# Kernel optimization log

Hardware: AMD Instinct MI355X
Metric: run time of the kernel (lower is better)

## Reference

```python
import jax, jax.numpy as jnp
import numpy as np

B, N, C, H = 16, 1024, 768, 12
GRID = 32  # 32x32 patch grid -> N = 1024 tokens
ROPE_BASE = 10000.0


def setup_inputs() -> dict:
    key = jax.random.key(0)
    k1, k2, k3 = jax.random.split(key, 3)
    x = jax.random.normal(k1, (B, N, C), dtype=jnp.float32)
    W_qkv = jax.random.normal(k2, (C, 3 * C), dtype=jnp.float32) * 0.02
    b_qkv = jnp.zeros((3 * C,), dtype=jnp.float32)
    W_proj = jax.random.normal(k3, (C, C), dtype=jnp.float32) * 0.02
    b_proj = jnp.zeros((C,), dtype=jnp.float32)
    ids = jnp.arange(N)
    pos_h = jnp.broadcast_to(ids // GRID, (B, N)).astype(jnp.int32)
    pos_w = jnp.broadcast_to(ids % GRID, (B, N)).astype(jnp.int32)
    return dict(x=x, W_qkv=W_qkv, b_qkv=b_qkv, W_proj=W_proj, b_proj=b_proj,
                pos_h=pos_h, pos_w=pos_w, num_heads=H)


def _rotate_half(t):
    t1, t2 = jnp.split(t, 2, axis=-1)
    return jnp.concatenate((-t2, t1), axis=-1)


def _rope_1d(t, pos, inv):
    # t: (B,H,N,d_rope), pos: (B,N), inv: (d_rope//2,)
    p = pos.astype(jnp.float32)[..., None] * inv      # (B,N,d_rope//2)
    p = p[:, None]                                    # (B,1,N,d_rope//2)
    cos = jnp.repeat(jnp.cos(p), 2, axis=-1)          # repeat_interleave(2)
    sin = jnp.repeat(jnp.sin(p), 2, axis=-1)
    return t * cos + _rotate_half(t) * sin


def reference(x, W_qkv, b_qkv, W_proj, b_proj, pos_h, pos_w, num_heads):
    Bx, Nx, Cx = x.shape
    hd = Cx // num_heads
    d_rope = hd // 2
    inv = 1.0 / ROPE_BASE ** (jnp.arange(0, d_rope, 2, dtype=jnp.float32) / float(max(d_rope, 1)))
    qkv = (x @ W_qkv + b_qkv).reshape(Bx, Nx, 3, num_heads, hd).transpose(2, 0, 3, 1, 4)
    q, k, v = qkv[0], qkv[1], qkv[2]                  # each (B,H,N,hd)
    # 2D RoPE: row-half / col-half of head_dim
    qh, qw = jnp.split(q, 2, axis=-1)
    kh, kw = jnp.split(k, 2, axis=-1)
    qh = _rope_1d(qh, pos_h, inv); kh = _rope_1d(kh, pos_h, inv)
    qw = _rope_1d(qw, pos_w, inv); kw = _rope_1d(kw, pos_w, inv)
    q = jnp.concatenate((qh, qw), axis=-1)
    k = jnp.concatenate((kh, kw), axis=-1)
    scale = hd ** -0.5
    attn = jax.nn.softmax(jnp.einsum('bhnd,bhmd->bhnm', q, k) * scale, axis=-1)
    out = jnp.einsum('bhnm,bhmd->bhnd', attn, v).transpose(0, 2, 1, 3).reshape(Bx, Nx, Cx)
    return out @ W_proj + b_proj
```

## Files before the change

### kernel.cpp

```cpp
#include <hip/hip_runtime.h>
#include <hip/hip_bf16.h>

#define B_ 16
#define N_ 1024
#define C_ 768
#define H_ 12
#define HD_ 64
#define QC_ (3*C_)

using bf16 = __hip_bfloat16;
using bf16x8 = __attribute__((ext_vector_type(8))) __bf16;
using f32x4  = __attribute__((ext_vector_type(4))) float;

__device__ __forceinline__ float tof(bf16 v){ return __bfloat162float(v); }

__device__ __forceinline__ void gload16(const void* g, void* l) {
  __builtin_amdgcn_global_load_lds(
      (const __attribute__((address_space(1))) unsigned int*)g,
      (__attribute__((address_space(3))) unsigned int*)l, 16, 0, 0);
}

__device__ __forceinline__ int xcd_swizzle(int bid, int nwg) {
  return (bid & 7) * (nwg >> 3) + (bid >> 3);
}

__device__ __forceinline__ unsigned pk2(float a, float b) {
  unsigned ua = (unsigned)__bfloat16_as_ushort(__float2bfloat16(a));
  unsigned ub = (unsigned)__bfloat16_as_ushort(__float2bfloat16(b));
  return ua | (ub << 16);
}

__global__ __launch_bounds__(256) void detect_dtype(
    const unsigned* __restrict__ x32, int* __restrict__ flag)
{
  __shared__ int cnt;
  if (threadIdx.x == 0) cnt = 0;
  __syncthreads();
  int local = 0;
  #pragma unroll
  for (int i = 0; i < 16; i++) {
    unsigned u = x32[threadIdx.x * 16 + i * 4096];
    unsigned e = (u >> 7) & 0xFF;
    local += (e >= 110 && e <= 140) ? 1 : 0;
  }
  atomicAdd(&cnt, local);
  __syncthreads();
  if (threadIdx.x == 0) *flag = (cnt > 2048) ? 1 : 0;
}

__global__ __launch_bounds__(256) void cvt_x(
    const void* __restrict__ x, bf16* __restrict__ xb,
    const int* __restrict__ flag, const int n4, const int off4)
{
  const int i = blockIdx.x * 256 + threadIdx.x;
  if (i >= n4) return;
  if (*flag) {
    ((uint2*)xb)[i] = ((const uint2*)x)[off4 + i];
  } else {
    float4 v = ((const float4*)x)[off4 + i];
    xb[i*4+0] = __float2bfloat16(v.x);
    xb[i*4+1] = __float2bfloat16(v.y);
    xb[i*4+2] = __float2bfloat16(v.z);
    xb[i*4+3] = __float2bfloat16(v.w);
  }
}

__global__ __launch_bounds__(256) void wt_cvt(
    const void* __restrict__ W, bf16* __restrict__ WT,
    const int K, const int Nd, const int* __restrict__ flag)
{
  __shared__ float t[32][33];
  const int fl = *flag;
  const int n0 = blockIdx.x * 32, k0 = blockIdx.y * 32;
  const int tx = threadIdx.x & 31, ty = threadIdx.x >> 5;
  for (int kk = ty; kk < 32; kk += 8) {
    const size_t gi = (size_t)(k0 + kk) * Nd + (n0 + tx);
    t[kk][tx] = fl ? tof(((const bf16*)W)[gi]) : ((const float*)W)[gi];
  }
  __syncthreads();
  for (int nn = ty; nn < 32; nn += 8)
    WT[(size_t)(n0 + nn) * K + (k0 + tx)] = __float2bfloat16(t[tx][nn]);
}

__global__ __launch_bounds__(256) void gemm_qkv_rope(
    const bf16* __restrict__ Ab, const bf16* __restrict__ WT,
    const void* __restrict__ bias, bf16* __restrict__ Qp,
    bf16* __restrict__ Kp, bf16* __restrict__ Vtb,
    const int* __restrict__ flag,
    const int* __restrict__ pos_h, const int* __restrict__ pos_w)
{
  const int K = C_;
  const bool bbf = (*flag != 0);

  __shared__ __align__(16) char smem[36864];
  unsigned short* As = (unsigned short*)smem;
  unsigned short* Bs = (unsigned short*)(smem + 16384);

  const int tid = threadIdx.x;
  const int l   = tid & 63;
  const int w   = tid >> 6;
  const int wm  = (w & 1) * 64;
  const int wn  = (w >> 1) * 64;

  const int nwg = gridDim.x * gridDim.y;
  const int bid = blockIdx.y * gridDim.x + blockIdx.x;
  const int lb  = xcd_swizzle(bid, nwg);
  const int gy  = gridDim.y;
  const int brow = lb / gy;
  const int bcol = lb - brow * gy;
  const int row0 = brow * 128;
  const int col0 = bcol * 128;

  const int srow = w*8 + (l >> 3);
  const int sch  = (l & 7) ^ (l >> 3);
  const bf16* Ast = Ab + (size_t)(row0 + srow) * K + sch * 8;
  const bf16* Bst = WT + (size_t)(col0 + srow) * K + sch * 8;

  f32x4 acc[4][4] = {};

  for (int k0 = 0; k0 < K; k0 += 64) {
    __syncthreads();
    #pragma unroll
    for (int i = 0; i < 4; i++) {
      gload16(Ast + (size_t)i*32*K + k0, As + (i*32 + w*8)*64);
      gload16(Bst + (size_t)i*32*K + k0, Bs + (i*32 + w*8)*64);
    }
    __syncthreads();
    #pragma unroll
    for (int s = 0; s < 2; s++) {
      bf16x8 af[4], bg[4];
      const int ch = (s*4 + (l >> 4)) ^ (l & 7);
      #pragma unroll
      for (int i = 0; i < 4; i++) {
        const int rowm = wm + i*16 + (l & 15);
        const int rown = wn + i*16 + (l & 15);
        af[i] = *(const bf16x8*)&As[rowm*64 + ch*8];
        bg[i] = *(const bf16x8*)&Bs[rown*64 + ch*8];
      }
      #pragma unroll
      for (int i = 0; i < 4; i++)
        #pragma unroll
        for (int j = 0; j < 4; j++)
          acc[i][j] = __builtin_amdgcn_mfma_f32_16x16x32_bf16(
                          af[i], bg[j], acc[i][j], 0, 0, 0);
    }
  }

  const int colbase = col0 + wn;
  const int t   = colbase / 768;
  const int h   = (colbase % 768) >> 6;
  const int dd0 = l & 15;
  float bv4[4];
  #pragma unroll
  for (int j = 0; j < 4; j++) {
    const int c = colbase + dd0 + j*16;
    bv4[j] = bbf ? tof(((const bf16*)bias)[c]) : ((const float*)bias)[c];
  }
  const int rb = row0 + wm + (l >> 4) * 4;

  __syncthreads();
  bf16* Ts = (bf16*)(smem + w * 9216);

  if (t == 2) {
    #pragma unroll
    for (int i = 0; i < 4; i++) {
      #pragma unroll
      for (int v = 0; v < 4; v++) {
        const int nl = i*16 + ((l >> 4) << 2) + v;
        #pragma unroll
        for (int j = 0; j < 4; j++) {
          const int dl = dd0 + j*16;
          const float y = acc[i][j][v] + bv4[j];
          Ts[dl*72 + (((nl >> 3) ^ (dl & 7)) << 3) + (nl & 7)] =
              __float2bfloat16(y);
        }
      }
    }
  } else {
    const int fi  = dd0 >> 1;
    const float LOG2B = 13.287712379549449f;
    const float f1 = exp2f(-LOG2B * (float)fi       * (1.0f/16.0f));
    const float f2 = exp2f(-LOG2B * (float)(fi + 8) * (1.0f/16.0f));
    #pragma unroll
    for (int i = 0; i < 4; i++) {
      #pragma unroll
      for (int v = 0; v < 4; v++) {
        const int r  = rb + i*16 + v;
        const int rl = i*16 + (l >> 4)*4 + v;
        float y0 = acc[i][0][v] + bv4[0];
        float y1 = acc[i][1][v] + bv4[1];
        float y2 = acc[i][2][v] + bv4[2];
        float y3 = acc[i][3][v] + bv4[3];
        const float ph = (float)pos_h[r];
        const float pw = (float)pos_w[r];
        float s1,c1,s2,c2,s3,c3,s4,c4;
        __sincosf(ph*f1, &s1, &c1);
        __sincosf(ph*f2, &s2, &c2);
        __sincosf(pw*f1, &s3, &c3);
        __sincosf(pw*f2, &s4, &c4);
        float z[4];
        z[0] = y0*c1 - y1*s1;
        z[1] = y1*c2 + y0*s2;
        z[2] = y2*c3 - y3*s3;
        z[3] = y3*c4 + y2*s4;
        if (t == 0) {
          const float QS = 0.18033688011112042f;
          z[0]*=QS; z[1]*=QS; z[2]*=QS; z[3]*=QS;
        }
        #pragma unroll
        for (int j = 0; j < 4; j++) {
          const int cl = dd0 + j*16;
          Ts[rl*72 + (((cl >> 3) ^ (rl & 7)) << 3) + (cl & 7)] =
              __float2bfloat16(z[j]);
        }
      }
    }
  }
  __syncthreads();

  if (t == 2) {
    const int n0 = (row0 + wm) & 1023;
    const int bp = (row0 + wm) >> 10;
    const size_t gbase = (size_t)(bp*12 + h) * 65536;
    #pragma unroll
    for (int dr = 0; dr < 8; dr++) {
      const int dl = dr*8 + (l >> 3);
      const int c  = l & 7;
      uint4 vv = *(const uint4*)&Ts[dl*72 + ((c ^ (dl & 7)) << 3)];
      *(uint4*)&Vtb[gbase + (size_t)dl*1024 + n0 + c*8] = vv;
    }
  } else {
    bf16* dst = (t == 0) ? Qp : Kp;
    const int rg0 = row0 + wm;
    const int bp  = rg0 >> 10;
    const int nb  = rg0 & 1023;
    const size_t gbase = (size_t)(bp*12 + h) * 65536;
    #pragma unroll
    for (int dr = 0; dr < 8; dr++) {
      const int rl = dr*8 + (l >> 3);
      const int c  = l & 7;
      uint4 vv = *(const uint4*)&Ts[rl*72 + ((c ^ (rl & 7)) << 3)];
      *(uint4*)&dst[gbase + (size_t)(nb + rl)*64 + c*8] = vv;
    }
  }
}

__global__ __launch_bounds__(256) void attn_mfma(
    const bf16* __restrict__ Qp, const bf16* __restrict__ Kp,
    const bf16* __restrict__ Vtb, bf16* __restrict__ ao)
{
  __shared__ __align__(16) bf16 QPs[64*64];
  __shared__ __align__(16) bf16 Ks[64*64];
  __shared__ __align__(16) bf16 Vs[64*64];
  bf16* Qs = QPs;
  bf16* Ps = QPs;
  const int tid = threadIdx.x;
  const int l   = tid & 63;
  const int w   = tid >> 6;

  const int nwg = gridDim.x * gridDim.y;
  const int bid = blockIdx.y * gridDim.x + blockIdx.x;
  const int lb  = xcd_swizzle(bid, nwg);
  const int qt  = lb & 15;
  const int bh  = lb >> 4;
  const size_t base = (size_t)bh * 65536;

  const int srow = w*8 + (l >> 3);
  const int sch  = (l & 7) ^ (l >> 3);
  const bf16* Qst = Qp  + base + (size_t)(qt*64 + srow)*64 + sch*8;
  const bf16* Kst = Kp  + base + (size_t)srow*64   + sch*8;
  const bf16* Vst = Vtb + base + (size_t)srow*1024 + sch*8;

  #pragma unroll
  for (int i = 0; i < 2; i++)
    gload16(Qst + (size_t)i*32*64, Qs + (i*32 + w*8)*64);
  __syncthreads();

  bf16x8 af[2];
  {
    const int row = w*16 + (l & 15);
    #pragma unroll
    for (int s = 0; s < 2; s++) {
      const int ch = (s*4 + (l >> 4)) ^ (row & 7);
      af[s] = *(const bf16x8*)&Qs[row*64 + ch*8];
    }
  }

  bf16x8 ones;
  #pragma unroll
  for (int i = 0; i < 8; i++) ones[i] = (__bf16)1.0f;

  float m_i = -3.0e38f;
  f32x4 l_acc = {};
  f32x4 o[4] = {};

  const int g    = l >> 4;
  const int qrow = w*16 + (l & 15);

  for (int kt = 0; kt < 16; kt++) {
    __syncthreads();
    #pragma unroll
    for (int i = 0; i < 2; i++) {
      gload16(Kst + (size_t)(kt*64 + i*32)*64, Ks + (i*32 + w*8)*64);
      gload16(Vst + (size_t)i*32*1024 + kt*64, Vs + (i*32 + w*8)*64);
    }
    __syncthreads();

    f32x4 s[4];
    __builtin_amdgcn_s_setprio(1);
    #pragma unroll
    for (int nt = 0; nt < 4; nt++) {
      f32x4 a = {};
      const int nrow = nt*16 + (l & 15);
      #pragma unroll
      for (int ss = 0; ss < 2; ss++) {
        const int ch = (ss*4 + (l >> 4)) ^ (nrow & 7);
        bf16x8 bg = *(const bf16x8*)&Ks[nrow*64 + ch*8];
        a = __builtin_amdgcn_mfma_f32_16x16x32_bf16(bg, af[ss], a, 0, 0, 0);
      }
      s[nt] = a;
    }
    __builtin_amdgcn_s_setprio(0);

    float a0 = fmaxf(fmaxf(s[0][0], s[0][1]), s[0][2]);
    float a1 = fmaxf(fmaxf(s[0][3], s[1][0]), s[1][1]);
    float a2 = fmaxf(fmaxf(s[1][2], s[1][3]), s[2][0]);
    float a3 = fmaxf(fmaxf(s[2][1], s[2][2]), s[2][3]);
    float a4 = fmaxf(fmaxf(s[3][0], s[3][1]), s[3][2]);
    float b0 = fmaxf(fmaxf(a0, a1), a2);
    float b1 = fmaxf(fmaxf(a3, a4), s[3][3]);
    float mloc = fmaxf(b0, b1);
    mloc = fmaxf(mloc, __shfl_xor(mloc, 16));
    const float m0 = fmaxf(mloc, __shfl_xor(mloc, 32));

    if (!__all(m0 - m_i <= 8.0f)) {
      const float mx = fmaxf(m_i, m0);
      const float alpha = exp2f(m_i - mx);
      m_i = mx;
      float a_o[4];
      #pragma unroll
      for (int v = 0; v < 4; v++)
        a_o[v] = __shfl(alpha, (l & 48) | ((g << 2) + v));
      #pragma unroll
      for (int v = 0; v < 4; v++) {
        l_acc[v] *= a_o[v];
        #pragma unroll
        for (int nt = 0; nt < 4; nt++) o[nt][v] *= a_o[v];
      }
    }

    #pragma unroll
    for (int nt = 0; nt < 4; nt++) {
      const float p0 = exp2f(s[nt][0] - m_i);
      const float p1 = exp2f(s[nt][1] - m_i);
      const float p2 = exp2f(s[nt][2] - m_i);
      const float p3 = exp2f(s[nt][3] - m_i);
      const int k0 = nt*16 + (g << 2);
      const int ch = (k0 >> 3) ^ (qrow & 7);
      uint2 uu;
      uu.x = pk2(p0, p1);
      uu.y = pk2(p2, p3);
      *(uint2*)&Ps[qrow*64 + ch*8 + (k0 & 7)] = uu;
    }

    __builtin_amdgcn_s_setprio(1);
    #pragma unroll
    for (int ss = 0; ss < 2; ss++) {
      const int pch  = (ss*4 + g) ^ (qrow & 7);
      bf16x8 pa = *(const bf16x8*)&Ps[qrow*64 + pch*8];
      l_acc = __builtin_amdgcn_mfma_f32_16x16x32_bf16(pa, ones, l_acc, 0,0,0);
      #pragma unroll
      for (int ntd = 0; ntd < 4; ntd++) {
        const int drow = ntd*16 + (l & 15);
        const int vch  = (ss*4 + (l >> 4)) ^ (drow & 7);
        bf16x8 vb = *(const bf16x8*)&Vs[drow*64 + vch*8];
        o[ntd] = __builtin_amdgcn_mfma_f32_16x16x32_bf16(pa, vb, o[ntd], 0,0,0);
      }
    }
    __builtin_amdgcn_s_setprio(0);
  }

  const int b = bh / 12, h = bh - b*12;
  #pragma unroll
  for (int v = 0; v < 4; v++) {
    const float invv = 1.0f / l_acc[v];
    const int rl = g*4 + v;
    #pragma unroll
    for (int ntd = 0; ntd < 4; ntd++) {
      const int cl = ntd*16 + (l & 15);
      Ps[(w*16 + rl)*64 + (((cl >> 3) ^ (rl & 7)) << 3) + (cl & 7)] =
          __float2bfloat16(o[ntd][v] * invv);
    }
  }
  #pragma unroll
  for (int e = 0; e < 2; e++) {
    const int rl = e*8 + (l >> 3);
    const int c  = l & 7;
    uint4 vv = *(const uint4*)&Ps[(w*16 + rl)*64 + ((c ^ (rl & 7)) << 3)];
    const int r = qt*64 + w*16 + rl;
    *(uint4*)&ao[((size_t)(b*1024 + r)) * 768 + h*64 + c*8] = vv;
  }
}

__global__ __launch_bounds__(256) void gemm_mfma(
    const bf16* __restrict__ Ab, const bf16* __restrict__ WT,
    const void* __restrict__ bias, void* __restrict__ Cout,
    const int Nd, const int K, const int c_row_off,
    const int* __restrict__ flag, const int bias_mode, const int c_mode)
{
  const int fl = *flag;
  const bool bbf = (bias_mode == 2) ? (fl != 0) : (bias_mode != 0);
  const bool cbf = (c_mode == 2) ? (fl != 0) : (c_mode != 0);

  __shared__ __align__(16) unsigned short As[128*64];
  __shared__ __align__(16) unsigned short Bs[128*64];

  const int tid = threadIdx.x;
  const int l   = tid & 63;
  const int w   = tid >> 6;
  const int wm  = (w & 1) * 64;
  const int wn  = (w >> 1) * 64;

  const int nwg = gridDim.x * gridDim.y;
  const int bid = blockIdx.y * gridDim.x + blockIdx.x;
  const int lb  = xcd_swizzle(bid, nwg);
  const int gy  = gridDim.y;
  const int brow = lb / gy;
  const int bcol = lb - brow * gy;
  const int row0 = brow * 128;
  const int col0 = bcol * 128;

  const int srow = w*8 + (l >> 3);
  const int sch  = (l & 7) ^ (l >> 3);
  const bf16* Ast = Ab + (size_t)(row0 + srow) * K + sch * 8;
  const bf16* Bst = WT + (size_t)(col0 + srow) * K + sch * 8;

  f32x4 acc[4][4] = {};

  for (int k0 = 0; k0 < K; k0 += 64) {
    __syncthreads();
    #pragma unroll
    for (int i = 0; i < 4; i++) {
      gload16(Ast + (size_t)i*32*K + k0, As + (i*32 + w*8)*64);
      gload16(Bst + (size_t)i*32*K + k0, Bs + (i*32 + w*8)*64);
    }
    __syncthreads();
    #pragma unroll
    for (int s = 0; s < 2; s++) {
      bf16x8 af[4], bg[4];
      const int ch = (s*4 + (l >> 4)) ^ (l & 7);
      #pragma unroll
      for (int i = 0; i < 4; i++) {
        const int rowm = wm + i*16 + (l & 15);
        const int rown = wn + i*16 + (l & 15);
        af[i] = *(const bf16x8*)&As[rowm*64 + ch*8];
        bg[i] = *(const bf16x8*)&Bs[rown*64 + ch*8];
      }
      #pragma unroll
      for (int i = 0; i < 4; i++)
        #pragma unroll
        for (int j = 0; j < 4; j++)
          acc[i][j] = __builtin_amdgcn_mfma_f32_16x16x32_bf16(
                          af[i], bg[j], acc[i][j], 0, 0, 0);
    }
  }

  const int cn    = col0 + wn + (l & 15);
  const int rbase = c_row_off + row0 + wm + (l >> 4) * 4;
  #pragma unroll
  for (int j = 0; j < 4; j++) {
    const int col = cn + j*16;
    const float bval = bbf ? tof(((const bf16*)bias)[col])
                           : ((const float*)bias)[col];
    #pragma unroll
    for (int i = 0; i < 4; i++) {
      #pragma unroll
      for (int v = 0; v < 4; v++) {
        const size_t r = (size_t)(rbase + i*16 + v);
        const float val = acc[i][j][v] + bval;
        if (cbf) ((bf16*)Cout)[r * Nd + col] = __float2bfloat16(val);
        else     ((float*)Cout)[r * Nd + col] = val;
      }
    }
  }
}

extern "C" void kernel_launch(void* const* d_in, const int* in_sizes, int n_in,
                              void* d_out, int out_size, void* d_ws, size_t ws_size,
                              hipStream_t stream)
{
  (void)in_sizes; (void)n_in; (void)out_size;
  const void* x     = d_in[0];
  const void* Wqkv  = d_in[1];
  const void* bqkv  = d_in[2];
  const void* Wproj = d_in[3];
  const void* bproj = d_in[4];
  const int*  pos_h = (const int*)d_in[5];
  const int*  pos_w = (const int*)d_in[6];

  int* flag = (int*)d_ws;
  char* p = (char*)d_ws + 256;
  bf16* WqkvT  = (bf16*)p; p += (size_t)QC_ * C_ * 2;
  bf16* WprojT = (bf16*)p; p += (size_t)C_ * C_ * 2;

  const size_t fixed = 256 + (size_t)QC_*C_*2 + (size_t)C_*C_*2;
  const size_t perb  = 5 * (size_t)N_ * C_ * 2;
  int CB = 16;
  if (ws_size < fixed + 16*perb) CB = 8;
  if (ws_size < fixed + 8*perb)  CB = 4;
  if (ws_size < fixed + 4*perb)  CB = 2;
  if (ws_size < fixed + 2*perb)  CB = 1;
  const int Mc = CB * N_;
  const size_t tsz = (size_t)Mc * C_;

  bf16* xb  = (bf16*)p;
  bf16* Qp  = xb  + tsz;
  bf16* Kp  = Qp  + tsz;
  bf16* Vtb = Kp  + tsz;
  bf16* ao  = Vtb + tsz;

  detect_dtype<<<1, 256, 0, stream>>>((const unsigned*)x, flag);
  wt_cvt<<<dim3(QC_/32, C_/32), 256, 0, stream>>>(Wqkv, WqkvT, C_, QC_, flag);
  wt_cvt<<<dim3(C_/32,  C_/32), 256, 0, stream>>>(Wproj, WprojT, C_, C_, flag);

  for (int c0 = 0; c0 < B_; c0 += CB) {
    const int n4 = Mc * C_ / 4;
    cvt_x<<<(n4 + 255)/256, 256, 0, stream>>>(x, xb, flag, n4, c0 * N_ * C_ / 4);
    gemm_qkv_rope<<<dim3(Mc/128, QC_/128), 256, 0, stream>>>(
        xb, WqkvT, bqkv, Qp, Kp, Vtb, flag,
        pos_h + (size_t)c0*N_, pos_w + (size_t)c0*N_);
    attn_mfma<<<dim3(N_/64, CB*H_), 256, 0, stream>>>(Qp, Kp, Vtb, ao);
    gemm_mfma<<<dim3(Mc/128, C_/128), 256, 0, stream>>>(
        ao, WprojT, bproj, d_out, C_, C_, c0*N_, flag, 2, 2);
  }
}
```

Baseline: 359.4 us.

## Double-buffer K/V tiles in attention kernel with async LDS prefetch

The attention kernel now keeps two LDS buffers each for K and V and prefetches the tile two iterations ahead with global_load_lds. The two full syncthreads per iteration are replaced by vmcnt waits and raw s_barrier calls. The goal is to hide global-memory latency behind the MFMA and softmax work. In exchange LDS use grows from 24KB to 40KB, which may lower occupancy, and the hand-written vmcnt counts are brittle if other loads get reordered.

```diff
diff --git a/kernel.cpp b/kernel.cpp
--- a/kernel.cpp
+++ b/kernel.cpp
@@ -250,8 +250,8 @@
     const bf16* __restrict__ Vtb, bf16* __restrict__ ao)
 {
   __shared__ __align__(16) bf16 QPs[64*64];
-  __shared__ __align__(16) bf16 Ks[64*64];
-  __shared__ __align__(16) bf16 Vs[64*64];
+  __shared__ __align__(16) bf16 Ks[2][64*64];
+  __shared__ __align__(16) bf16 Vs[2][64*64];
   bf16* Qs = QPs;
   bf16* Ps = QPs;
   const int tid = threadIdx.x;
@@ -271,9 +271,16 @@
   const bf16* Kst = Kp  + base + (size_t)srow*64   + sch*8;
   const bf16* Vst = Vtb + base + (size_t)srow*1024 + sch*8;
 
+  #define STAGE_KV(tt, b)                                                    \
+    { gload16(Kst + (size_t)((tt)*64 +  0)*64, Ks[b] + ( 0 + w*8)*64);       \
+      gload16(Kst + (size_t)((tt)*64 + 32)*64, Ks[b] + (32 + w*8)*64);       \
+      gload16(Vst + (size_t)(tt)*64,           Vs[b] + ( 0 + w*8)*64);       \
+      gload16(Vst + (size_t)32*1024 + (tt)*64, Vs[b] + (32 + w*8)*64); }
+
   #pragma unroll
   for (int i = 0; i < 2; i++)
     gload16(Qst + (size_t)i*32*64, Qs + (i*32 + w*8)*64);
+  STAGE_KV(0, 0);
   __syncthreads();
 
   bf16x8 af[2];
@@ -285,6 +292,7 @@
       af[s] = *(const bf16x8*)&Qs[row*64 + ch*8];
     }
   }
+  STAGE_KV(1, 1);
 
   bf16x8 ones;
   #pragma unroll
@@ -298,13 +306,15 @@
   const int qrow = w*16 + (l & 15);
 
   for (int kt = 0; kt < 16; kt++) {
-    __syncthreads();
-    #pragma unroll
-    for (int i = 0; i < 2; i++) {
-      gload16(Kst + (size_t)(kt*64 + i*32)*64, Ks + (i*32 + w*8)*64);
-      gload16(Vst + (size_t)i*32*1024 + kt*64, Vs + (i*32 + w*8)*64);
-    }
-    __syncthreads();
+    const int cur = kt & 1;
+    if (kt > 0) {
+      if (kt < 15) { asm volatile("s_waitcnt vmcnt(4)" ::: "memory"); }
+      else         { asm volatile("s_waitcnt vmcnt(0)" ::: "memory"); }
+      __builtin_amdgcn_s_barrier();
+      asm volatile("" ::: "memory");
+    }
+    const bf16* Ksb = Ks[cur];
+    const bf16* Vsb = Vs[cur];
 
     f32x4 s[4];
     __builtin_amdgcn_s_setprio(1);
@@ -315,7 +325,7 @@
       #pragma unroll
       for (int ss = 0; ss < 2; ss++) {
         const int ch = (ss*4 + (l >> 4)) ^ (nrow & 7);
-        bf16x8 bg = *(const bf16x8*)&Ks[nrow*64 + ch*8];
+        bf16x8 bg = *(const bf16x8*)&Ksb[nrow*64 + ch*8];
         a = __builtin_amdgcn_mfma_f32_16x16x32_bf16(bg, af[ss], a, 0, 0, 0);
       }
       s[nt] = a;
@@ -373,12 +383,18 @@
       for (int ntd = 0; ntd < 4; ntd++) {
         const int drow = ntd*16 + (l & 15);
         const int vch  = (ss*4 + (l >> 4)) ^ (drow & 7);
-        bf16x8 vb = *(const bf16x8*)&Vs[drow*64 + vch*8];
+        bf16x8 vb = *(const bf16x8*)&Vsb[drow*64 + vch*8];
         o[ntd] = __builtin_amdgcn_mfma_f32_16x16x32_bf16(pa, vb, o[ntd], 0,0,0);
       }
     }
     __builtin_amdgcn_s_setprio(0);
-  }
+
+    asm volatile("" ::: "memory");
+    __builtin_amdgcn_s_barrier();
+    asm volatile("" ::: "memory");
+    if (kt + 2 < 16) STAGE_KV(kt + 2, cur);
+  }
+  #undef STAGE_KV
 
   const int b = bh / 12, h = bh - b*12;
   #pragma unroll
```

Result: faster. 348.5 us (-3.0%).

## Load attention Q/K/V fragments directly from global, widen blocks to 128 queries

Applied to the files above, without the earlier changes.

The attention kernel no longer stages K and V tiles through LDS with __syncthreads barriers. Each wave now loads its MFMA fragments for Q, K and V straight from global memory, relying on L1/L2 for reuse across waves. Blocks grow to 512 threads covering 128 query rows, and LDS is kept only for the P tile and the output transpose. This removes barriers and LDS traffic, but adds more global load instructions with less coalesced, scattered accesses, and load latency is now exposed in the inner loop.

```diff
diff --git a/kernel.cpp b/kernel.cpp
--- a/kernel.cpp
+++ b/kernel.cpp
@@ -245,15 +245,11 @@
   }
 }
 
-__global__ __launch_bounds__(256) void attn_mfma(
+__global__ __launch_bounds__(512, 4) void attn_mfma(
     const bf16* __restrict__ Qp, const bf16* __restrict__ Kp,
     const bf16* __restrict__ Vtb, bf16* __restrict__ ao)
 {
-  __shared__ __align__(16) bf16 QPs[64*64];
-  __shared__ __align__(16) bf16 Ks[64*64];
-  __shared__ __align__(16) bf16 Vs[64*64];
-  bf16* Qs = QPs;
-  bf16* Ps = QPs;
+  __shared__ __align__(16) bf16 Ps[128*64];
   const int tid = threadIdx.x;
   const int l   = tid & 63;
   const int w   = tid >> 6;
@@ -261,30 +257,18 @@
   const int nwg = gridDim.x * gridDim.y;
   const int bid = blockIdx.y * gridDim.x + blockIdx.x;
   const int lb  = xcd_swizzle(bid, nwg);
-  const int qt  = lb & 15;
-  const int bh  = lb >> 4;
+  const int qt  = lb & 7;
+  const int bh  = lb >> 3;
   const size_t base = (size_t)bh * 65536;
 
-  const int srow = w*8 + (l >> 3);
-  const int sch  = (l & 7) ^ (l >> 3);
-  const bf16* Qst = Qp  + base + (size_t)(qt*64 + srow)*64 + sch*8;
-  const bf16* Kst = Kp  + base + (size_t)srow*64   + sch*8;
-  const bf16* Vst = Vtb + base + (size_t)srow*1024 + sch*8;
-
-  #pragma unroll
-  for (int i = 0; i < 2; i++)
-    gload16(Qst + (size_t)i*32*64, Qs + (i*32 + w*8)*64);
-  __syncthreads();
+  const int g    = l >> 4;
+  const int qrow = w*16 + (l & 15);
 
   bf16x8 af[2];
-  {
-    const int row = w*16 + (l & 15);
-    #pragma unroll
-    for (int s = 0; s < 2; s++) {
-      const int ch = (s*4 + (l >> 4)) ^ (row & 7);
-      af[s] = *(const bf16x8*)&Qs[row*64 + ch*8];
-    }
-  }
+  #pragma unroll
+  for (int s = 0; s < 2; s++)
+    af[s] = *(const bf16x8*)(Qp + base +
+                (size_t)(qt*128 + qrow)*64 + (s*4 + g)*8);
 
   bf16x8 ones;
   #pragma unroll
@@ -294,30 +278,25 @@
   f32x4 l_acc = {};
   f32x4 o[4] = {};
 
-  const int g    = l >> 4;
-  const int qrow = w*16 + (l & 15);
+  const bf16* Kb = Kp  + base + (size_t)(l & 15)*64 + g*8;
+  const bf16* Vb = Vtb + base + (size_t)(l & 15)*1024 + g*8;
 
   for (int kt = 0; kt < 16; kt++) {
-    __syncthreads();
-    #pragma unroll
-    for (int i = 0; i < 2; i++) {
-      gload16(Kst + (size_t)(kt*64 + i*32)*64, Ks + (i*32 + w*8)*64);
-      gload16(Vst + (size_t)i*32*1024 + kt*64, Vs + (i*32 + w*8)*64);
-    }
-    __syncthreads();
+    bf16x8 kf[4][2];
+    #pragma unroll
+    for (int nt = 0; nt < 4; nt++)
+      #pragma unroll
+      for (int ss = 0; ss < 2; ss++)
+        kf[nt][ss] = *(const bf16x8*)(Kb +
+            (size_t)(kt*64 + nt*16)*64 + ss*32);
 
     f32x4 s[4];
     __builtin_amdgcn_s_setprio(1);
     #pragma unroll
     for (int nt = 0; nt < 4; nt++) {
       f32x4 a = {};
-      const int nrow = nt*16 + (l & 15);
-      #pragma unroll
-      for (int ss = 0; ss < 2; ss++) {
-        const int ch = (ss*4 + (l >> 4)) ^ (nrow & 7);
-        bf16x8 bg = *(const bf16x8*)&Ks[nrow*64 + ch*8];
-        a = __builtin_amdgcn_mfma_f32_16x16x32_bf16(bg, af[ss], a, 0, 0, 0);
-      }
+      a = __builtin_amdgcn_mfma_f32_16x16x32_bf16(kf[nt][0], af[0], a, 0,0,0);
+      a = __builtin_amdgcn_mfma_f32_16x16x32_bf16(kf[nt][1], af[1], a, 0,0,0);
       s[nt] = a;
     }
     __builtin_amdgcn_s_setprio(0);
@@ -371,9 +350,8 @@
       l_acc = __builtin_amdgcn_mfma_f32_16x16x32_bf16(pa, ones, l_acc, 0,0,0);
       #pragma unroll
       for (int ntd = 0; ntd < 4; ntd++) {
-        const int drow = ntd*16 + (l & 15);
-        const int vch  = (ss*4 + (l >> 4)) ^ (drow & 7);
-        bf16x8 vb = *(const bf16x8*)&Vs[drow*64 + vch*8];
+        bf16x8 vb = *(const bf16x8*)(Vb +
+            (size_t)(ntd*16)*1024 + kt*64 + ss*32);
         o[ntd] = __builtin_amdgcn_mfma_f32_16x16x32_bf16(pa, vb, o[ntd], 0,0,0);
       }
     }
@@ -397,7 +375,7 @@
     const int rl = e*8 + (l >> 3);
     const int c  = l & 7;
     uint4 vv = *(const uint4*)&Ps[(w*16 + rl)*64 + ((c ^ (rl & 7)) << 3)];
-    const int r = qt*64 + w*16 + rl;
+    const int r = qt*128 + w*16 + rl;
     *(uint4*)&ao[((size_t)(b*1024 + r)) * 768 + h*64 + c*8] = vv;
   }
 }
@@ -529,7 +507,7 @@
     gemm_qkv_rope<<<dim3(Mc/128, QC_/128), 256, 0, stream>>>(
         xb, WqkvT, bqkv, Qp, Kp, Vtb, flag,
         pos_h + (size_t)c0*N_, pos_w + (size_t)c0*N_);
-    attn_mfma<<<dim3(N_/64, CB*H_), 256, 0, stream>>>(Qp, Kp, Vtb, ao);
+    attn_mfma<<<dim3(N_/128, CB*H_), 512, 0, stream>>>(Qp, Kp, Vtb, ao);
     gemm_mfma<<<dim3(Mc/128, C_/128), 256, 0, stream>>>(
         ao, WprojT, bproj, d_out, C_, C_, c0*N_, flag, 2, 2);
   }
```

After: 581.0 us. 61.7% more time.
